# Kernel optimization log

Hardware: AMD Instinct MI355X
Metric: run time of the kernel (lower is better)

The kernel has to match this reference:

```python
import jax, jax.numpy as jnp
import numpy as np

N_TOKENS = 16384
D_MODEL = 1024
N_SEG = 4
H_SEG = 1024  # intermediate_size (4096) // num_segments


def setup_inputs() -> dict:
    key = jax.random.key(0)
    kx, ki, kg, ku, kd = jax.random.split(key, 5)
    x = jax.random.normal(kx, (N_TOKENS, D_MODEL), dtype=jnp.float32)
    token_segment_indices = jax.random.randint(ki, (N_TOKENS,), 0, N_SEG, dtype=jnp.int64)
    s = 1.0 / np.sqrt(D_MODEL)
    # weights stored [seg, in, out] for x @ W
    gate_w = jax.random.normal(kg, (N_SEG, D_MODEL, H_SEG), dtype=jnp.float32) * s
    up_w = jax.random.normal(ku, (N_SEG, D_MODEL, H_SEG), dtype=jnp.float32) * s
    down_w = jax.random.normal(kd, (N_SEG, H_SEG, D_MODEL), dtype=jnp.float32) * (1.0 / np.sqrt(H_SEG))
    return {
        'x': x,
        'gate_w': gate_w,
        'up_w': up_w,
        'down_w': down_w,
        'token_segment_indices': token_segment_indices,
    }


def reference(x, gate_w, up_w, down_w, token_segment_indices):
    # _forward_with_indices: each token is processed only by its assigned
    # segment's SwiGLU FFN; all other contributions are zero.  We compute each
    # segment densely and mask (jit-friendly, same math as gather->ffn->scatter).
    out = jnp.zeros_like(x)
    for s in range(N_SEG):
        hidden = jax.nn.silu(x @ gate_w[s]) * (x @ up_w[s])  # [N, H_SEG]
        y = hidden @ down_w[s]                                # [N, D_MODEL]
        mask = (token_segment_indices == s)[:, None]
        out = out + jnp.where(mask, y, 0.0)
    return out
```

## Files before the change

kernel.cpp:

```cpp
#include <hip/hip_runtime.h>
#include <hip/hip_bf16.h>
#include <math.h>

#define NT   16384
#define DM   1024
#define NSEG 4
#define BK   64
#define HS   1024
#define TBLN 68

typedef __attribute__((ext_vector_type(8))) short bf16x8;
typedef __attribute__((ext_vector_type(4))) float f32x4;

typedef __attribute__((address_space(1))) unsigned int gu32;
typedef __attribute__((address_space(3))) unsigned int lu32;

__device__ __forceinline__ void gll16(const void* g, void* l) {
  __builtin_amdgcn_global_load_lds((gu32*)(unsigned long long)g,
                                   (lu32*)(unsigned int)(unsigned long long)l,
                                   16, 0, 0);
}

__device__ __forceinline__ unsigned short cvt_bf16(float f) {
  unsigned int u = __float_as_uint(f);
  u += 0x7fffu + ((u >> 16) & 1u);
  return (unsigned short)(u >> 16);
}

__global__ __launch_bounds__(256) void k_prepw(
    const int* __restrict__ idx, int* __restrict__ part,
    const float* __restrict__ gw, const float* __restrict__ uw, const float* __restrict__ dw,
    unsigned short* __restrict__ gwt, unsigned short* __restrict__ uwt,
    unsigned short* __restrict__ dwt) {
  __shared__ float tile[64][65];
  const int bid = blockIdx.x, tid = threadIdx.x;
  if (bid < 64) {
    __shared__ int sc[5];
    if (tid < 5) sc[tid] = 0;
    __syncthreads();
    int lane = tid & 63;
    int w32 = idx[bid * 256 + tid];
    unsigned long long m = __ballot((tid & 1) && (w32 != 0));
    if (lane == 0 && m) atomicAdd(&sc[4], 1);
    __syncthreads();
    int is32 = (sc[4] != 0);
    int s = w32;
    if (!is32) s = idx[bid * 512 + 2 * tid];
#pragma unroll
    for (int q = 0; q < 4; ++q) {
      m = __ballot(s == q);
      if (lane == 0 && m) atomicAdd(&sc[q], (int)__popcll(m));
    }
    __syncthreads();
    if (tid < 4) part[bid * 8 + tid] = sc[tid];
    if (tid == 4) part[bid * 8 + 4] = is32;
    return;
  }
  int tb = bid - 64;
  int mtx = tb >> 10, seg = (tb >> 8) & 3, tl = tb & 255;
  const float* src = (mtx == 0 ? gw : mtx == 1 ? uw : dw) + (size_t)seg * DM * HS;
  unsigned short* dst = (mtx == 0 ? gwt : mtx == 1 ? uwt : dwt) + (size_t)seg * DM * HS;
  int n0 = (tl & 15) * 64, k0 = (tl >> 4) * 64;
  int col = tid & 63, rb = tid >> 6;
#pragma unroll
  for (int i = 0; i < 64; i += 4)
    tile[i + rb][col] = src[(size_t)(k0 + i + rb) * 1024 + n0 + col];
  __syncthreads();
  int kp = tid & 31, nb = tid >> 5;
#pragma unroll
  for (int j = 0; j < 64; j += 8) {
    int nn = j + nb;
    unsigned int w = (unsigned)cvt_bf16(tile[2 * kp][nn]) |
                     ((unsigned)cvt_bf16(tile[2 * kp + 1][nn]) << 16);
    *(unsigned int*)(dst + (size_t)(n0 + nn) * 1024 + k0 + 2 * kp) = w;
  }
}

__global__ __launch_bounds__(256) void k_cvtrank(
    const int* __restrict__ idx, const int* __restrict__ part,
    const float4* __restrict__ x,
    int* __restrict__ meta, int2* __restrict__ table,
    int* __restrict__ perm, uint4* __restrict__ xc) {
  __shared__ int cnt[64][4];
  __shared__ int wsum[4][4];
  __shared__ int tot[4], pref[4], gbase[4];
  __shared__ int rnk8[8];
  __shared__ int flag_s;
  const int tid = threadIdx.x, bid = blockIdx.x;
  const int lane = tid & 63, wv = tid >> 6;
  const int c = bid >> 5;
  const int p0 = (bid & 31) * 8;

  if (tid == 0) flag_s = part[c * 8 + 4];
  if (wv == 0) {
#pragma unroll
    for (int s = 0; s < 4; ++s) cnt[lane][s] = part[lane * 8 + s];
  }
  __syncthreads();
  const int is32 = flag_s;
  int tok = c * 256 + tid;
  int s_t = is32 ? idx[tok] : idx[2 * tok];
  int myr = 0;
  unsigned long long lt = (1ull << lane) - 1;
#pragma unroll
  for (int q = 0; q < 4; ++q) {
    unsigned long long m = __ballot(s_t == q);
    if (lane == 0) wsum[wv][q] = (int)__popcll(m);
    if (s_t == q) myr = (int)__popcll(m & lt);
  }
  __syncthreads();
  if (tid < 4) {
    int s = tid, t = 0, p = 0;
    for (int b = 0; b < 64; ++b) { if (b == c) p = t; t += cnt[b][s]; }
    tot[s] = t; pref[s] = p;
  }
  __syncthreads();
  if (tid == 0) {
    gbase[0] = 0;
    for (int s = 1; s < 4; ++s) gbase[s] = gbase[s - 1] + tot[s - 1];
    if (bid == 0) {
      int nt = 0;
      for (int s = 0; s < 4; ++s) {
        meta[s] = tot[s]; meta[5 + s] = gbase[s];
        for (int m0 = 0; m0 < tot[s]; m0 += 256) table[nt++] = make_int2(s, m0);
      }
      for (; nt < TBLN; ++nt) table[nt] = make_int2(-1, 0);
    }
  }
  __syncthreads();
  int wpre = 0;
  for (int w2 = 0; w2 < wv; ++w2) wpre += wsum[w2][s_t];
  int r = gbase[s_t] + pref[s_t] + wpre + myr;
  if (tid >= p0 && tid < p0 + 8) {
    perm[r] = tok;
    rnk8[tid - p0] = r;
  }
  __syncthreads();
  const int j = tid >> 5, l2 = tid & 31;
  const int tok8 = bid * 8 + j;
  const float4* src = x + (size_t)tok8 * 256;
  uint4* dst = xc + (size_t)rnk8[j] * 128;
#pragma unroll
  for (int it = 0; it < 4; ++it) {
    float4 a = src[it * 64 + l2 * 2];
    float4 b = src[it * 64 + l2 * 2 + 1];
    uint4 o;
    o.x = cvt_bf16(a.x) | ((unsigned)cvt_bf16(a.y) << 16);
    o.y = cvt_bf16(a.z) | ((unsigned)cvt_bf16(a.w) << 16);
    o.z = cvt_bf16(b.x) | ((unsigned)cvt_bf16(b.y) << 16);
    o.w = cvt_bf16(b.z) | ((unsigned)cvt_bf16(b.w) << 16);
    dst[it * 32 + l2] = o;
  }
}

#define WAITBAR_(N) \
  asm volatile("s_waitcnt vmcnt(" #N ") lgkmcnt(0)\n\ts_barrier" ::: "memory")
#define WAITBAR(N) WAITBAR_(N)

#define LDF(BUF, CUR, RB, F)                                               \
  F[0][0] = *(const bf16x8*)(&BUF[CUR][((RB) + fm) * 64] + x0);            \
  F[0][1] = *(const bf16x8*)(&BUF[CUR][((RB) + fm) * 64] + x1);            \
  F[1][0] = *(const bf16x8*)(&BUF[CUR][((RB) + 16 + fm) * 64] + x0);       \
  F[1][1] = *(const bf16x8*)(&BUF[CUR][((RB) + 16 + fm) * 64] + x1);

#define MM8(ACC, MH, NH, AF, BF)                                                                                            \
  __builtin_amdgcn_s_setprio(1);                                                                                            \
  ACC[2*(MH)+0][2*(NH)+0] = __builtin_amdgcn_mfma_f32_16x16x32_bf16(AF[0][0], BF[0][0], ACC[2*(MH)+0][2*(NH)+0], 0, 0, 0);  \
  ACC[2*(MH)+0][2*(NH)+1] = __builtin_amdgcn_mfma_f32_16x16x32_bf16(AF[0][0], BF[1][0], ACC[2*(MH)+0][2*(NH)+1], 0, 0, 0);  \
  ACC[2*(MH)+1][2*(NH)+0] = __builtin_amdgcn_mfma_f32_16x16x32_bf16(AF[1][0], BF[0][0], ACC[2*(MH)+1][2*(NH)+0], 0, 0, 0);  \
  ACC[2*(MH)+1][2*(NH)+1] = __builtin_amdgcn_mfma_f32_16x16x32_bf16(AF[1][0], BF[1][0], ACC[2*(MH)+1][2*(NH)+1], 0, 0, 0);  \
  ACC[2*(MH)+0][2*(NH)+0] = __builtin_amdgcn_mfma_f32_16x16x32_bf16(AF[0][1], BF[0][1], ACC[2*(MH)+0][2*(NH)+0], 0, 0, 0);  \
  ACC[2*(MH)+0][2*(NH)+1] = __builtin_amdgcn_mfma_f32_16x16x32_bf16(AF[0][1], BF[1][1], ACC[2*(MH)+0][2*(NH)+1], 0, 0, 0);  \
  ACC[2*(MH)+1][2*(NH)+0] = __builtin_amdgcn_mfma_f32_16x16x32_bf16(AF[1][1], BF[0][1], ACC[2*(MH)+1][2*(NH)+0], 0, 0, 0);  \
  ACC[2*(MH)+1][2*(NH)+1] = __builtin_amdgcn_mfma_f32_16x16x32_bf16(AF[1][1], BF[1][1], ACC[2*(MH)+1][2*(NH)+1], 0, 0, 0);  \
  __builtin_amdgcn_s_setprio(0);

__global__ __launch_bounds__(512) void k_gateup(
    const unsigned short* __restrict__ xc,
    const unsigned short* __restrict__ gwt,
    const unsigned short* __restrict__ uwt,
    const int* __restrict__ meta,
    const int2* __restrict__ table,
    unsigned short* __restrict__ hidden) {
  __shared__ __align__(16) unsigned short As[3][256 * BK];
  __shared__ __align__(16) unsigned short Bg[3][64 * BK];
  __shared__ __align__(16) unsigned short Bu[3][64 * BK];
  const int bid = blockIdx.x, tid = threadIdx.x;
  const int2 te = table[bid >> 4];
  if (te.x < 0) return;
  const int seg = te.x, m0 = te.y;
  const int count = meta[seg], base = meta[5 + seg];
  const int n0 = (bid & 15) * 64;

  const int lane = tid & 63;
  const int wv = tid >> 6;
  const int l0 = lane >> 3, j = lane & 7;

  const int rl0 = wv * 8, rl1 = 64 + wv * 8;
  const int rb0 = (rl0 & 31) + (rl0 >> 5) * 64;
  const int rb1 = (rl1 & 31) + (rl1 >> 5) * 64;
  const int a0d0 = rb0 * 128, a0d1 = rb1 * 128;
  const int a1d0 = a0d0 + 32 * 128, a1d1 = a0d1 + 32 * 128;
  const int r00 = rb0 + l0, r01 = rb1 + l0;
  const int r10 = r00 + 32, r11 = r01 + 32;
  auto rowof = [&](int r) { int g = m0 + r; return g < count ? g : count - 1; };
  const unsigned short* a0p0 = xc + (size_t)(base + rowof(r00)) * DM + (j ^ (r00 & 7)) * 8;
  const unsigned short* a0p1 = xc + (size_t)(base + rowof(r01)) * DM + (j ^ (r01 & 7)) * 8;
  const unsigned short* a1p0 = xc + (size_t)(base + rowof(r10)) * DM + (j ^ (r10 & 7)) * 8;
  const unsigned short* a1p1 = xc + (size_t)(base + rowof(r11)) * DM + (j ^ (r11 & 7)) * 8;
  const int nb = wv * 8 + l0;
  const unsigned short* gp  = gwt + (size_t)(seg * HS + n0 + nb) * DM + (j ^ (nb & 7)) * 8;
  const unsigned short* upp = uwt + (size_t)(seg * HS + n0 + nb) * DM + (j ^ (nb & 7)) * 8;
  const int bd = wv * 1024;

  const int wm = (wv & 3) * 64;
  const int wn = (wv >> 2) * 32;
  const int fm = lane & 15, fq = lane >> 4;
  const int x0 = (fq ^ (fm & 7)) * 8;
  const int x1 = ((4 + fq) ^ (fm & 7)) * 8;

  f32x4 accg[4][2] = {};
  f32x4 accu[4][2] = {};

#define GU_STAGE(B) {                                         \
    gll16(a0p0, (char*)&As[B][0] + a0d0);                     \
    gll16(a0p1, (char*)&As[B][0] + a0d1);                     \
    gll16(gp,   (char*)&Bg[B][0] + bd);                       \
    gll16(upp,  (char*)&Bu[B][0] + bd);                       \
    gll16(a1p0, (char*)&As[B][0] + a1d0);                     \
    gll16(a1p1, (char*)&As[B][0] + a1d1);                     \
    a0p0 += BK; a0p1 += BK; a1p0 += BK; a1p1 += BK; gp += BK; upp += BK; \
  }

#define GU_ITER(C, P) {                                       \
    bf16x8 af[2][2], af2[2][2], bg2[2][2], bu2[2][2];         \
    gll16(a0p0, (char*)&As[P][0] + a0d0);                     \
    gll16(a0p1, (char*)&As[P][0] + a0d1);                     \
    WAITBAR(11);                                              \
    LDF(As, C, wm, af); LDF(Bg, C, wn, bg2);                  \
    MM8(accg, 0, 0, af, bg2);                                 \
    gll16(gp, (char*)&Bg[P][0] + bd);                         \
    WAITBAR(11);                                              \
    LDF(Bu, C, wn, bu2);                                      \
    MM8(accu, 0, 0, af, bu2);                                 \
    gll16(upp, (char*)&Bu[P][0] + bd);                        \
    WAITBAR(10);                                              \
    LDF(As, C, wm + 32, af2);                                 \
    MM8(accg, 1, 0, af2, bg2);                                \
    gll16(a1p0, (char*)&As[P][0] + a1d0);                     \
    gll16(a1p1, (char*)&As[P][0] + a1d1);                     \
    MM8(accu, 1, 0, af2, bu2);                                \
    a0p0 += BK; a0p1 += BK; a1p0 += BK; a1p1 += BK; gp += BK; upp += BK; \
  }

#define GU_EPI(C, W1, W2, W3) {                               \
    bf16x8 af[2][2], af2[2][2], bg2[2][2], bu2[2][2];         \
    WAITBAR(W1);                                              \
    LDF(As, C, wm, af); LDF(Bg, C, wn, bg2);                  \
    MM8(accg, 0, 0, af, bg2);                                 \
    WAITBAR(W2);                                              \
    LDF(Bu, C, wn, bu2);                                      \
    MM8(accu, 0, 0, af, bu2);                                 \
    WAITBAR(W3);                                              \
    LDF(As, C, wm + 32, af2);                                 \
    MM8(accg, 1, 0, af2, bg2);                                \
    MM8(accu, 1, 0, af2, bu2);                                \
  }

  GU_STAGE(0);
  GU_STAGE(1);

#pragma unroll 1
  for (int g3 = 0; g3 < 4; ++g3) {
    GU_ITER(0, 2); GU_ITER(1, 0); GU_ITER(2, 1);
  }
  GU_ITER(0, 2);
  GU_ITER(1, 0);
  GU_EPI(2, 9, 8, 6);
  GU_EPI(0, 3, 2, 0);
#undef GU_ITER
#undef GU_EPI
#undef GU_STAGE

  const int rq = fq * 4;
#pragma unroll
  for (int mi = 0; mi < 4; ++mi) {
#pragma unroll
    for (int r = 0; r < 4; ++r) {
      int row = m0 + wm + mi * 16 + rq + r;
      if (row < count) {
        unsigned short* h = hidden + (size_t)(base + row) * HS + n0 + wn;
#pragma unroll
        for (int ni = 0; ni < 2; ++ni) {
          float gv = accg[mi][ni][r];
          float uv = accu[mi][ni][r];
          float sig = 1.0f / (1.0f + __expf(-gv));
          h[ni * 16 + fm] = cvt_bf16(gv * sig * uv);
        }
      }
    }
  }
}

__global__ __launch_bounds__(512) void k_down(
    const unsigned short* __restrict__ hidden,
    const unsigned short* __restrict__ dwt,
    const int* __restrict__ meta,
    const int2* __restrict__ table,
    const int* __restrict__ perm,
    float* __restrict__ out) {
  __shared__ __align__(16) unsigned short As[3][256 * BK];
  __shared__ __align__(16) unsigned short Bs[3][128 * BK];
  const int bid = blockIdx.x, tid = threadIdx.x;
  const int2 te = table[bid >> 3];
  if (te.x < 0) return;
  const int seg = te.x, m0 = te.y;
  const int count = meta[seg], base = meta[5 + seg];
  const int n0 = (bid & 7) * 128;

  const int lane = tid & 63;
  const int wv = tid >> 6;
  const int l0 = lane >> 3, j = lane & 7;

  const int rl0 = wv * 8, rl1 = 64 + wv * 8;
  const int rb0 = (rl0 & 31) + (rl0 >> 5) * 64;
  const int rb1 = (rl1 & 31) + (rl1 >> 5) * 64;
  const int a0d0 = rb0 * 128, a0d1 = rb1 * 128;
  const int a1d0 = a0d0 + 32 * 128, a1d1 = a0d1 + 32 * 128;
  const int r00 = rb0 + l0, r01 = rb1 + l0;
  const int r10 = r00 + 32, r11 = r01 + 32;
  auto rowof = [&](int r) { int g = m0 + r; return g < count ? g : count - 1; };
  const unsigned short* a0p0 = hidden + (size_t)(base + rowof(r00)) * HS + (j ^ (r00 & 7)) * 8;
  const unsigned short* a0p1 = hidden + (size_t)(base + rowof(r01)) * HS + (j ^ (r01 & 7)) * 8;
  const unsigned short* a1p0 = hidden + (size_t)(base + rowof(r10)) * HS + (j ^ (r10 & 7)) * 8;
  const unsigned short* a1p1 = hidden + (size_t)(base + rowof(r11)) * HS + (j ^ (r11 & 7)) * 8;
  const int nl = wv * 8 + l0;
  const int nb0 = (nl & 31) + (nl >> 5) * 64;
  const int nb1 = nb0 + 32;
  const unsigned short* bp0 = dwt + (size_t)(seg * DM + n0 + nb0) * HS + (j ^ (nb0 & 7)) * 8;
  const unsigned short* bp1 = dwt + (size_t)(seg * DM + n0 + nb1) * HS + (j ^ (nb1 & 7)) * 8;
  const int bw = wv * 8;
  const int bd0 = ((bw & 31) + (bw >> 5) * 64) * 128;
  const int bd1 = bd0 + 32 * 128;

  const int wm = (wv & 3) * 64;
  const int wn = (wv >> 2) * 64;
  const int fm = lane & 15, fq = lane >> 4;
  const int x0 = (fq ^ (fm & 7)) * 8;
  const int x1 = ((4 + fq) ^ (fm & 7)) * 8;

  f32x4 acc[4][4] = {};

#define DN_STAGE(B) {                                         \
    gll16(a0p0, (char*)&As[B][0] + a0d0);                     \
    gll16(a0p1, (char*)&As[B][0] + a0d1);                     \
    gll16(bp0,  (char*)&Bs[B][0] + bd0);                      \
    gll16(bp1,  (char*)&Bs[B][0] + bd1);                      \
    gll16(a1p0, (char*)&As[B][0] + a1d0);                     \
    gll16(a1p1, (char*)&As[B][0] + a1d1);                     \
    a0p0 += BK; a0p1 += BK; a1p0 += BK; a1p1 += BK; bp0 += BK; bp1 += BK; \
  }

#define DN_ITER(C, P) {                                       \
    bf16x8 af[2][2], af2[2][2], b0[2][2], b1[2][2];           \
    gll16(a0p0, (char*)&As[P][0] + a0d0);                     \
    gll16(a0p1, (char*)&As[P][0] + a0d1);                     \
    WAITBAR(11);                                              \
    LDF(As, C, wm, af); LDF(Bs, C, wn, b0);                   \
    MM8(acc, 0, 0, af, b0);                                   \
    gll16(bp0, (char*)&Bs[P][0] + bd0);                       \
    WAITBAR(11);                                              \
    LDF(Bs, C, wn + 32, b1);                                  \
    MM8(acc, 0, 1, af, b1);                                   \
    gll16(bp1, (char*)&Bs[P][0] + bd1);                       \
    WAITBAR(10);                                              \
    LDF(As, C, wm + 32, af2);                                 \
    MM8(acc, 1, 0, af2, b0);                                  \
    gll16(a1p0, (char*)&As[P][0] + a1d0);                     \
    gll16(a1p1, (char*)&As[P][0] + a1d1);                     \
    MM8(acc, 1, 1, af2, b1);                                  \
    a0p0 += BK; a0p1 += BK; a1p0 += BK; a1p1 += BK; bp0 += BK; bp1 += BK; \
  }

#define DN_EPI(C, W1, W2, W3) {                               \
    bf16x8 af[2][2], af2[2][2], b0[2][2], b1[2][2];           \
    WAITBAR(W1);                                              \
    LDF(As, C, wm, af); LDF(Bs, C, wn, b0);                   \
    MM8(acc, 0, 0, af, b0);                                   \
    WAITBAR(W2);                                              \
    LDF(Bs, C, wn + 32, b1);                                  \
    MM8(acc, 0, 1, af, b1);                                   \
    WAITBAR(W3);                                              \
    LDF(As, C, wm + 32, af2);                                 \
    MM8(acc, 1, 0, af2, b0);                                  \
    MM8(acc, 1, 1, af2, b1);                                  \
  }

  DN_STAGE(0);
  DN_STAGE(1);

#pragma unroll 1
  for (int g3 = 0; g3 < 4; ++g3) {
    DN_ITER(0, 2); DN_ITER(1, 0); DN_ITER(2, 1);
  }
  DN_ITER(0, 2);
  DN_ITER(1, 0);
  DN_EPI(2, 9, 8, 6);
  DN_EPI(0, 3, 2, 0);
#undef DN_ITER
#undef DN_EPI
#undef DN_STAGE

  const int rq = fq * 4;
#pragma unroll
  for (int mi = 0; mi < 4; ++mi) {
#pragma unroll
    for (int r = 0; r < 4; ++r) {
      int row = m0 + wm + mi * 16 + rq + r;
      if (row < count) {
        int t = perm[base + row];
        float* o = out + (size_t)t * DM + n0 + wn;
#pragma unroll
        for (int ni = 0; ni < 4; ++ni)
          o[ni * 16 + fm] = acc[mi][ni][r];
      }
    }
  }
}


extern "C" void kernel_launch(void* const* d_in, const int* in_sizes, int n_in,
                              void* d_out, int out_size, void* d_ws, size_t ws_size,
                              hipStream_t stream) {
  const float* x  = (const float*)d_in[0];
  const float* gw = (const float*)d_in[1];
  const float* uw = (const float*)d_in[2];
  const float* dw = (const float*)d_in[3];
  const int* tsi  = (const int*)d_in[4];
  float* out = (float*)d_out;

  char* ws = (char*)d_ws;
  int*  meta  = (int*)ws;
  int*  part  = (int*)(ws + 256);
  int2* table = (int2*)(ws + 4096);
  int*  perm  = (int*)(ws + 8192);
  unsigned short* xc  = (unsigned short*)(ws + (1 << 18));
  unsigned short* gwt = xc + (size_t)NT * DM;
  unsigned short* uwt = gwt + (size_t)NSEG * HS * DM;
  unsigned short* dwt = uwt + (size_t)NSEG * HS * DM;
  unsigned short* hid = dwt + (size_t)NSEG * DM * HS;

  k_prepw<<<64 + 3072, 256, 0, stream>>>(tsi, part, gw, uw, dw, gwt, uwt, dwt);
  k_cvtrank<<<2048, 256, 0, stream>>>(tsi, part, (const float4*)x, meta, table, perm, (uint4*)xc);
  k_gateup<<<16 * TBLN, 512, 0, stream>>>(xc, gwt, uwt, meta, table, hid);
  k_down<<<8 * TBLN, 512, 0, stream>>>(hid, dwt, meta, table, perm, out);
}
```

Before: 312.2 us.

## Restructure GEMM main loops into barrier-separated load/compute phases with priority

New measurement: 316.7 us. About the same (+1.4%).

```diff
diff --git a/kernel.cpp b/kernel.cpp
--- a/kernel.cpp
+++ b/kernel.cpp
@@ -153,9 +153,12 @@
   }
 }
 
-#define WAITBAR_(N) \
-  asm volatile("s_waitcnt vmcnt(" #N ") lgkmcnt(0)\n\ts_barrier" ::: "memory")
-#define WAITBAR(N) WAITBAR_(N)
+#define SBAR() __builtin_amdgcn_s_barrier()
+#define W_LGKM() do { asm volatile("s_waitcnt lgkmcnt(0)" ::: "memory"); \
+                      __builtin_amdgcn_sched_barrier(0); } while (0)
+#define W_VM_LGKM_(N) do { asm volatile("s_waitcnt vmcnt(" #N ") lgkmcnt(0)" ::: "memory"); \
+                           __builtin_amdgcn_sched_barrier(0); } while (0)
+#define W_VM_LGKM(N) W_VM_LGKM_(N)
 
 #define LDF(BUF, CUR, RB, F)                                               \
   F[0][0] = *(const bf16x8*)(&BUF[CUR][((RB) + fm) * 64] + x0);            \
@@ -164,7 +167,6 @@
   F[1][1] = *(const bf16x8*)(&BUF[CUR][((RB) + 16 + fm) * 64] + x1);
 
 #define MM8(ACC, MH, NH, AF, BF)                                                                                            \
-  __builtin_amdgcn_s_setprio(1);                                                                                            \
   ACC[2*(MH)+0][2*(NH)+0] = __builtin_amdgcn_mfma_f32_16x16x32_bf16(AF[0][0], BF[0][0], ACC[2*(MH)+0][2*(NH)+0], 0, 0, 0);  \
   ACC[2*(MH)+0][2*(NH)+1] = __builtin_amdgcn_mfma_f32_16x16x32_bf16(AF[0][0], BF[1][0], ACC[2*(MH)+0][2*(NH)+1], 0, 0, 0);  \
   ACC[2*(MH)+1][2*(NH)+0] = __builtin_amdgcn_mfma_f32_16x16x32_bf16(AF[1][0], BF[0][0], ACC[2*(MH)+1][2*(NH)+0], 0, 0, 0);  \
@@ -172,8 +174,7 @@
   ACC[2*(MH)+0][2*(NH)+0] = __builtin_amdgcn_mfma_f32_16x16x32_bf16(AF[0][1], BF[0][1], ACC[2*(MH)+0][2*(NH)+0], 0, 0, 0);  \
   ACC[2*(MH)+0][2*(NH)+1] = __builtin_amdgcn_mfma_f32_16x16x32_bf16(AF[0][1], BF[1][1], ACC[2*(MH)+0][2*(NH)+1], 0, 0, 0);  \
   ACC[2*(MH)+1][2*(NH)+0] = __builtin_amdgcn_mfma_f32_16x16x32_bf16(AF[1][1], BF[0][1], ACC[2*(MH)+1][2*(NH)+0], 0, 0, 0);  \
-  ACC[2*(MH)+1][2*(NH)+1] = __builtin_amdgcn_mfma_f32_16x16x32_bf16(AF[1][1], BF[1][1], ACC[2*(MH)+1][2*(NH)+1], 0, 0, 0);  \
-  __builtin_amdgcn_s_setprio(0);
+  ACC[2*(MH)+1][2*(NH)+1] = __builtin_amdgcn_mfma_f32_16x16x32_bf16(AF[1][1], BF[1][1], ACC[2*(MH)+1][2*(NH)+1], 0, 0, 0);
 
 __global__ __launch_bounds__(512) void k_gateup(
     const unsigned short* __restrict__ xc,
@@ -232,54 +233,69 @@
     a0p0 += BK; a0p1 += BK; a1p0 += BK; a1p1 += BK; gp += BK; upp += BK; \
   }
 
-#define GU_ITER(C, P) {                                       \
+#define GU_TILE(C, PB) {                                      \
     bf16x8 af[2][2], af2[2][2], bg2[2][2], bu2[2][2];         \
-    gll16(a0p0, (char*)&As[P][0] + a0d0);                     \
-    gll16(a0p1, (char*)&As[P][0] + a0d1);                     \
-    WAITBAR(11);                                              \
-    LDF(As, C, wm, af); LDF(Bg, C, wn, bg2);                  \
+    LDF(As, C, wm, af);                                       \
+    LDF(Bg, C, wn, bg2);                                      \
+    LDF(Bu, C, wn, bu2);                                      \
+    gll16(a0p0, (char*)&As[PB][0] + a0d0);                    \
+    gll16(a0p1, (char*)&As[PB][0] + a0d1);                    \
+    gll16(gp,   (char*)&Bg[PB][0] + bd);                      \
+    SBAR(); W_LGKM();                                         \
+    __builtin_amdgcn_s_setprio(1);                            \
     MM8(accg, 0, 0, af, bg2);                                 \
-    gll16(gp, (char*)&Bg[P][0] + bd);                         \
-    WAITBAR(11);                                              \
-    LDF(Bu, C, wn, bu2);                                      \
     MM8(accu, 0, 0, af, bu2);                                 \
-    gll16(upp, (char*)&Bu[P][0] + bd);                        \
-    WAITBAR(10);                                              \
+    __builtin_amdgcn_s_setprio(0);                            \
+    SBAR();                                                   \
     LDF(As, C, wm + 32, af2);                                 \
-    MM8(accg, 1, 0, af2, bg2);                                \
-    gll16(a1p0, (char*)&As[P][0] + a1d0);                     \
-    gll16(a1p1, (char*)&As[P][0] + a1d1);                     \
-    MM8(accu, 1, 0, af2, bu2);                                \
-    a0p0 += BK; a0p1 += BK; a1p0 += BK; a1p1 += BK; gp += BK; upp += BK; \
-  }
-
-#define GU_EPI(C, W1, W2, W3) {                               \
-    bf16x8 af[2][2], af2[2][2], bg2[2][2], bu2[2][2];         \
-    WAITBAR(W1);                                              \
-    LDF(As, C, wm, af); LDF(Bg, C, wn, bg2);                  \
-    MM8(accg, 0, 0, af, bg2);                                 \
-    WAITBAR(W2);                                              \
-    LDF(Bu, C, wn, bu2);                                      \
-    MM8(accu, 0, 0, af, bu2);                                 \
-    WAITBAR(W3);                                              \
-    LDF(As, C, wm + 32, af2);                                 \
+    gll16(upp,  (char*)&Bu[PB][0] + bd);                      \
+    gll16(a1p0, (char*)&As[PB][0] + a1d0);                    \
+    gll16(a1p1, (char*)&As[PB][0] + a1d1);                    \
+    SBAR(); W_VM_LGKM(6);                                     \
+    __builtin_amdgcn_s_setprio(1);                            \
     MM8(accg, 1, 0, af2, bg2);                                \
     MM8(accu, 1, 0, af2, bu2);                                \
+    __builtin_amdgcn_s_setprio(0);                            \
+    SBAR();                                                   \
+    a0p0 += BK; a0p1 += BK; a1p0 += BK; a1p1 += BK; gp += BK; upp += BK; \
+  }
+
+#define GU_TILE_E(C, DOVM) {                                  \
+    bf16x8 af[2][2], af2[2][2], bg2[2][2], bu2[2][2];         \
+    LDF(As, C, wm, af);                                       \
+    LDF(Bg, C, wn, bg2);                                      \
+    LDF(Bu, C, wn, bu2);                                      \
+    SBAR(); W_LGKM();                                         \
+    __builtin_amdgcn_s_setprio(1);                            \
+    MM8(accg, 0, 0, af, bg2);                                 \
+    MM8(accu, 0, 0, af, bu2);                                 \
+    __builtin_amdgcn_s_setprio(0);                            \
+    SBAR();                                                   \
+    LDF(As, C, wm + 32, af2);                                 \
+    SBAR();                                                   \
+    if (DOVM) { W_VM_LGKM(0); } else { W_LGKM(); }            \
+    __builtin_amdgcn_s_setprio(1);                            \
+    MM8(accg, 1, 0, af2, bg2);                                \
+    MM8(accu, 1, 0, af2, bu2);                                \
+    __builtin_amdgcn_s_setprio(0);                            \
+    SBAR();                                                   \
   }
 
   GU_STAGE(0);
   GU_STAGE(1);
+  asm volatile("s_waitcnt vmcnt(6)" ::: "memory");
+  SBAR();
 
 #pragma unroll 1
   for (int g3 = 0; g3 < 4; ++g3) {
-    GU_ITER(0, 2); GU_ITER(1, 0); GU_ITER(2, 1);
-  }
-  GU_ITER(0, 2);
-  GU_ITER(1, 0);
-  GU_EPI(2, 9, 8, 6);
-  GU_EPI(0, 3, 2, 0);
-#undef GU_ITER
-#undef GU_EPI
+    GU_TILE(0, 2); GU_TILE(1, 0); GU_TILE(2, 1);
+  }
+  GU_TILE(0, 2);
+  GU_TILE(1, 0);
+  GU_TILE_E(2, 1);
+  GU_TILE_E(0, 0);
+#undef GU_TILE
+#undef GU_TILE_E
 #undef GU_STAGE
 
   const int rq = fq * 4;
@@ -361,54 +377,69 @@
     a0p0 += BK; a0p1 += BK; a1p0 += BK; a1p1 += BK; bp0 += BK; bp1 += BK; \
   }
 
-#define DN_ITER(C, P) {                                       \
+#define DN_TILE(C, PB) {                                      \
     bf16x8 af[2][2], af2[2][2], b0[2][2], b1[2][2];           \
-    gll16(a0p0, (char*)&As[P][0] + a0d0);                     \
-    gll16(a0p1, (char*)&As[P][0] + a0d1);                     \
-    WAITBAR(11);                                              \
-    LDF(As, C, wm, af); LDF(Bs, C, wn, b0);                   \
+    LDF(As, C, wm, af);                                       \
+    LDF(Bs, C, wn, b0);                                       \
+    LDF(Bs, C, wn + 32, b1);                                  \
+    gll16(a0p0, (char*)&As[PB][0] + a0d0);                    \
+    gll16(a0p1, (char*)&As[PB][0] + a0d1);                    \
+    gll16(bp0,  (char*)&Bs[PB][0] + bd0);                     \
+    SBAR(); W_LGKM();                                         \
+    __builtin_amdgcn_s_setprio(1);                            \
     MM8(acc, 0, 0, af, b0);                                   \
-    gll16(bp0, (char*)&Bs[P][0] + bd0);                       \
-    WAITBAR(11);                                              \
-    LDF(Bs, C, wn + 32, b1);                                  \
     MM8(acc, 0, 1, af, b1);                                   \
-    gll16(bp1, (char*)&Bs[P][0] + bd1);                       \
-    WAITBAR(10);                                              \
+    __builtin_amdgcn_s_setprio(0);                            \
+    SBAR();                                                   \
     LDF(As, C, wm + 32, af2);                                 \
-    MM8(acc, 1, 0, af2, b0);                                  \
-    gll16(a1p0, (char*)&As[P][0] + a1d0);                     \
-    gll16(a1p1, (char*)&As[P][0] + a1d1);                     \
-    MM8(acc, 1, 1, af2, b1);                                  \
-    a0p0 += BK; a0p1 += BK; a1p0 += BK; a1p1 += BK; bp0 += BK; bp1 += BK; \
-  }
-
-#define DN_EPI(C, W1, W2, W3) {                               \
-    bf16x8 af[2][2], af2[2][2], b0[2][2], b1[2][2];           \
-    WAITBAR(W1);                                              \
-    LDF(As, C, wm, af); LDF(Bs, C, wn, b0);                   \
-    MM8(acc, 0, 0, af, b0);                                   \
-    WAITBAR(W2);                                              \
-    LDF(Bs, C, wn + 32, b1);                                  \
-    MM8(acc, 0, 1, af, b1);                                   \
-    WAITBAR(W3);                                              \
-    LDF(As, C, wm + 32, af2);                                 \
+    gll16(bp1,  (char*)&Bs[PB][0] + bd1);                     \
+    gll16(a1p0, (char*)&As[PB][0] + a1d0);                    \
+    gll16(a1p1, (char*)&As[PB][0] + a1d1);                    \
+    SBAR(); W_VM_LGKM(6);                                     \
+    __builtin_amdgcn_s_setprio(1);                            \
     MM8(acc, 1, 0, af2, b0);                                  \
     MM8(acc, 1, 1, af2, b1);                                  \
+    __builtin_amdgcn_s_setprio(0);                            \
+    SBAR();                                                   \
+    a0p0 += BK; a0p1 += BK; a1p0 += BK; a1p1 += BK; bp0 += BK; bp1 += BK; \
+  }
+
+#define DN_TILE_E(C, DOVM) {                                  \
+    bf16x8 af[2][2], af2[2][2], b0[2][2], b1[2][2];           \
+    LDF(As, C, wm, af);                                       \
+    LDF(Bs, C, wn, b0);                                       \
+    LDF(Bs, C, wn + 32, b1);                                  \
+    SBAR(); W_LGKM();                                         \
+    __builtin_amdgcn_s_setprio(1);                            \
+    MM8(acc, 0, 0, af, b0);                                   \
+    MM8(acc, 0, 1, af, b1);                                   \
+    __builtin_amdgcn_s_setprio(0);                            \
+    SBAR();                                                   \
+    LDF(As, C, wm + 32, af2);                                 \
+    SBAR();                                                   \
+    if (DOVM) { W_VM_LGKM(0); } else { W_LGKM(); }            \
+    __builtin_amdgcn_s_setprio(1);                            \
+    MM8(acc, 1, 0, af2, b0);                                  \
+    MM8(acc, 1, 1, af2, b1);                                  \
+    __builtin_amdgcn_s_setprio(0);                            \
+    SBAR();                                                   \
   }
 
   DN_STAGE(0);
   DN_STAGE(1);
+  asm volatile("s_waitcnt vmcnt(6)" ::: "memory");
+  SBAR();
 
 #pragma unroll 1
   for (int g3 = 0; g3 < 4; ++g3) {
-    DN_ITER(0, 2); DN_ITER(1, 0); DN_ITER(2, 1);
-  }
-  DN_ITER(0, 2);
-  DN_ITER(1, 0);
-  DN_EPI(2, 9, 8, 6);
-  DN_EPI(0, 3, 2, 0);
-#undef DN_ITER
-#undef DN_EPI
+    DN_TILE(0, 2); DN_TILE(1, 0); DN_TILE(2, 1);
+  }
+  DN_TILE(0, 2);
+  DN_TILE(1, 0);
+  DN_TILE_E(2, 1);
+  DN_TILE_E(0, 0);
+#undef DN_TILE
+#undef DN_TILE_E
 #undef DN_STAGE
 
   const int rq = fq * 4;
```
